# Performance work log

Hardware: AMD Instinct MI355X
Metric: run time of the kernel (lower is better)

The kernel has to match this reference:

```python
import jax, jax.numpy as jnp
import numpy as np

N_NODES = 500000
FEAT_DIM = 128
BATCH = 50000
K = 16


def setup_inputs() -> dict:
    key = jax.random.key(0)
    k1, k2, k3 = jax.random.split(key, 3)
    features = jax.random.normal(k1, (N_NODES, FEAT_DIM), dtype=jnp.float32)
    # weights = pow(degree, beta); positive floats (uniform in (0.05, 1.05))
    neigh_w = jax.random.uniform(k2, (BATCH, K), dtype=jnp.float32) + 0.05
    neigh_idx = jax.random.randint(k3, (BATCH, K), 0, N_NODES, dtype=jnp.int64)
    return {"features": features, "neigh_w": neigh_w, "neigh_idx": neigh_idx}


def reference(features, neigh_w, neigh_idx):
    # Row-normalize weights (mask = mask.div(mask.sum(1, keepdim=True)))
    w = neigh_w / jnp.sum(neigh_w, axis=-1, keepdims=True)  # [B, K]
    # Gather neighbor embeddings (features(unique_nodes) + sparse mask rows)
    gathered = features[neigh_idx]  # [B, K, D]
    # mask.mm(embed_matrix) == weighted mean over sampled neighbors
    to_feats = jnp.einsum("bk,bkd->bd", w, gathered)  # [B, D]
    return to_feats
```

## Files before the change

kernel.cpp:

```cpp
#include <hip/hip_runtime.h>

#define KNEIGH 16
#define FDIM   128

typedef float f32x4 __attribute__((ext_vector_type(4)));

__global__ __launch_bounds__(256) void WeightedAggregator_89489938580183_kernel(
    const float* __restrict__ features,
    const float* __restrict__ neigh_w,
    const int*   __restrict__ neigh_idx,
    float*       __restrict__ out,
    int batch) {

    const int lane = threadIdx.x & 63;
    int row = blockIdx.x * (blockDim.x >> 6) + (threadIdx.x >> 6);
    if (row >= batch) return;
    row = __builtin_amdgcn_readfirstlane(row);

    const float* wp = neigh_w   + (size_t)row * KNEIGH;
    const int*   ip = neigh_idx + (size_t)row * KNEIGH;
    float w[KNEIGH];
    int   idx[KNEIGH];
    #pragma unroll
    for (int k = 0; k < KNEIGH; ++k) { w[k] = wp[k]; idx[k] = ip[k]; }

    float s = w[0];
    #pragma unroll
    for (int k = 1; k < KNEIGH; ++k) s += w[k];
    const float inv = 1.0f / s;

    const int half = lane >> 5;
    const int sub  = lane & 31;

    f32x4 acc0 = (f32x4)(0.0f);
    f32x4 acc1 = (f32x4)(0.0f);

    #pragma unroll
    for (int kk = 0; kk < KNEIGH; kk += 4) {
        const int   iA = half ? idx[kk + 1] : idx[kk];
        const float wA = (half ? w[kk + 1] : w[kk]) * inv;
        const int   iB = half ? idx[kk + 3] : idx[kk + 2];
        const float wB = (half ? w[kk + 3] : w[kk + 2]) * inv;

        const f32x4 fA = ((const f32x4*)features)[((unsigned)iA << 5) + sub];
        const f32x4 fB = ((const f32x4*)features)[((unsigned)iB << 5) + sub];

        acc0 += wA * fA;
        acc1 += wB * fB;
    }

    f32x4 acc = acc0 + acc1;

    acc.x += __shfl_xor(acc.x, 32);
    acc.y += __shfl_xor(acc.y, 32);
    acc.z += __shfl_xor(acc.z, 32);
    acc.w += __shfl_xor(acc.w, 32);

    if (half == 0) {
        f32x4* dst = (f32x4*)(out + (size_t)row * FDIM) + sub;
        __builtin_nontemporal_store(acc, dst);
    }
}

extern "C" void kernel_launch(void* const* d_in, const int* in_sizes, int n_in,
                              void* d_out, int out_size, void* d_ws, size_t ws_size,
                              hipStream_t stream) {
    const float* features  = (const float*)d_in[0];
    const float* neigh_w   = (const float*)d_in[1];
    const int*   neigh_idx = (const int*)d_in[2];
    float*       out       = (float*)d_out;

    const int batch = in_sizes[1] / KNEIGH;

    const int waves_per_block = 256 / 64;
    const int blocks = (batch + waves_per_block - 1) / waves_per_block;
    WeightedAggregator_89489938580183_kernel<<<blocks, 256, 0, stream>>>(
        features, neigh_w, neigh_idx, out, batch);
}
```

Measured before the change: 380.1 us.

## Map four rows per wavefront with 16-lane groups and shuffle-broadcast neighbors

Each wavefront now handles four output rows, one per 16-lane group. Each lane loads one weight and one index with a coalesced vector load, the normalization sum is a shuffle reduction, and neighbor entries are broadcast by shuffles. Each lane gathers two contiguous float4 per neighbor, which removes the cross-half reduction and the scalar per-row loads. The trade-off is 16 sequential gather steps per lane instead of 4 paired ones, and the output store is no longer nontemporal.

```diff
diff --git a/kernel.cpp b/kernel.cpp
--- a/kernel.cpp
+++ b/kernel.cpp
@@ -13,52 +13,48 @@
     int batch) {
 
     const int lane = threadIdx.x & 63;
-    int row = blockIdx.x * (blockDim.x >> 6) + (threadIdx.x >> 6);
-    if (row >= batch) return;
-    row = __builtin_amdgcn_readfirstlane(row);
+    int wid = blockIdx.x * (blockDim.x >> 6) + (threadIdx.x >> 6);
+    int r0 = wid * 4;
+    if (r0 >= batch) return;
+    r0 = __builtin_amdgcn_readfirstlane(r0);
 
-    const float* wp = neigh_w   + (size_t)row * KNEIGH;
-    const int*   ip = neigh_idx + (size_t)row * KNEIGH;
-    float w[KNEIGH];
-    int   idx[KNEIGH];
-    #pragma unroll
-    for (int k = 0; k < KNEIGH; ++k) { w[k] = wp[k]; idx[k] = ip[k]; }
+    const int g   = lane >> 4;
+    const int ell = lane & 15;
 
-    float s = w[0];
-    #pragma unroll
-    for (int k = 1; k < KNEIGH; ++k) s += w[k];
+    const int myrow = (r0 + g < batch) ? r0 + g : batch - 1;
+
+    const float wv = neigh_w  [(size_t)myrow * KNEIGH + ell];
+    const int   iv = neigh_idx[(size_t)myrow * KNEIGH + ell];
+
+    float s = wv;
+    s += __shfl_xor(s, 1);
+    s += __shfl_xor(s, 2);
+    s += __shfl_xor(s, 4);
+    s += __shfl_xor(s, 8);
     const float inv = 1.0f / s;
 
-    const int half = lane >> 5;
-    const int sub  = lane & 31;
+    const int gbase = lane & 48;
 
     f32x4 acc0 = (f32x4)(0.0f);
     f32x4 acc1 = (f32x4)(0.0f);
 
     #pragma unroll
-    for (int kk = 0; kk < KNEIGH; kk += 4) {
-        const int   iA = half ? idx[kk + 1] : idx[kk];
-        const float wA = (half ? w[kk + 1] : w[kk]) * inv;
-        const int   iB = half ? idx[kk + 3] : idx[kk + 2];
-        const float wB = (half ? w[kk + 3] : w[kk + 2]) * inv;
+    for (int k = 0; k < KNEIGH; ++k) {
+        const float wk = __shfl(wv, gbase + k) * inv;
+        const int   ik = __shfl(iv, gbase + k);
 
-        const f32x4 fA = ((const f32x4*)features)[((unsigned)iA << 5) + sub];
-        const f32x4 fB = ((const f32x4*)features)[((unsigned)iB << 5) + sub];
+        const unsigned off = ((unsigned)ik << 5) + (unsigned)(ell << 1);
+        const f32x4 f0 = ((const f32x4*)features)[off];
+        const f32x4 f1 = ((const f32x4*)features)[off + 1];
 
-        acc0 += wA * fA;
-        acc1 += wB * fB;
+        acc0 += wk * f0;
+        acc1 += wk * f1;
     }
 
-    f32x4 acc = acc0 + acc1;
-
-    acc.x += __shfl_xor(acc.x, 32);
-    acc.y += __shfl_xor(acc.y, 32);
-    acc.z += __shfl_xor(acc.z, 32);
-    acc.w += __shfl_xor(acc.w, 32);
-
-    if (half == 0) {
-        f32x4* dst = (f32x4*)(out + (size_t)row * FDIM) + sub;
-        __builtin_nontemporal_store(acc, dst);
+    if (r0 + g < batch) {
+        f32x4* dst = (f32x4*)out + ((size_t)(r0 + g) << 5) + (ell << 1);
+        dst[0] = acc0;
+        dst[1] = acc1;
     }
 }
 
@@ -72,8 +68,8 @@
 
     const int batch = in_sizes[1] / KNEIGH;
 
-    const int waves_per_block = 256 / 64;
-    const int blocks = (batch + waves_per_block - 1) / waves_per_block;
+    const int rows_per_block = 4 * (256 / 64);
+    const int blocks = (batch + rows_per_block - 1) / rows_per_block;
     WeightedAggregator_89489938580183_kernel<<<blocks, 256, 0, stream>>>(
         features, neigh_w, neigh_idx, out, batch);
 }
```

Result: slower. 400.6 us (+5.4%).
